# Kernel optimization log

Measured on AMD Instinct MI355X. Metric: run time of the kernel, lower is better.

Reference implementation:

```python
import jax, jax.numpy as jnp
import numpy as np

B, H, L = 8, 256, 8192

def setup_inputs() -> dict:
    key = jax.random.key(0)
    k1, k2, k3 = jax.random.split(key, 3)
    u = jax.random.normal(k1, (B, H, L), dtype=jnp.float32)
    K = jax.random.normal(k2, (H, L), dtype=jnp.float32)
    # D ~ uniform_ring with min=max=1.0, field='real' -> random signs on unit ring
    D = jnp.where(jax.random.uniform(k3, (H,)) < 0.5, -1.0, 1.0).astype(jnp.float32)
    return {"u": u, "K": K, "D": D}

def reference(u, K, D):
    # FFT-based circular long convolution per channel: y = ifft(fft(u) * fft(K)).real
    u_s = jnp.fft.fft(u, axis=-1)            # (B,H,L) complex
    k_s = jnp.fft.fft(K, axis=-1)            # (H,L)   complex
    y = jnp.fft.ifft(u_s * k_s[None], axis=-1).real  # (B,H,L)
    y = y + D[None, :, None] * u             # skip connection D*u
    y = jnp.tanh(y)
    return y
```

## Files before the change

### kernel.cpp

```cpp
#include <hip/hip_runtime.h>
#include <math.h>


#define LL 8192
#define NT 256
#define HH 256
#define TWO_PI 6.2831853071795864f
#define CP16 0.98078528040323f
#define SP16 0.19509032201613f
#define CP8  0.92387953251129f
#define SP8  0.38268343236509f

__device__ __forceinline__ int PHYS(int i) {
    return i ^ ((i >> 5) & 15) ^ (((i >> 8) & 1) << 4);
}
__device__ __forceinline__ float fast_tanh(float x) {
    float e = __expf(2.0f * x);
    return 1.0f - 2.0f / (e + 1.0f);
}

template<int JT>
__device__ __forceinline__ void fill_pyr_cs(float c0, float s0, float Er, float Ei,
                                            float* twr, float* twi) {
    const int off = (1 << JT) - 1;
    twr[off] = c0; twi[off] = s0;
    #pragma unroll
    for (int m = 1; m < (1 << JT); ++m) {
        const float pr = twr[off + m - 1], pi = twi[off + m - 1];
        twr[off + m] = pr * Er - pi * Ei;
        twi[off + m] = pr * Ei + pi * Er;
    }
    #pragma unroll
    for (int j = JT - 1; j >= 0; --j) {
        #pragma unroll
        for (int m = 0; m < (1 << j); ++m) {
            const float a = twr[(2 << j) - 1 + m], b = twi[(2 << j) - 1 + m];
            twr[(1 << j) - 1 + m] = a * a - b * b;
            twi[(1 << j) - 1 + m] = 2.0f * a * b;
        }
    }
}
template<int JT>
__device__ __forceinline__ void fill_pyr(float ang0, float Er, float Ei,
                                         float* twr, float* twi) {
    float s, c;
    __sincosf(ang0, &s, &c);
    fill_pyr_cs<JT>(c, s, Er, Ei, twr, twi);
}

template<int R2>
__device__ __forceinline__ void dif_apply(float* xr, float* xi,
                                          const float* twr, const float* twi) {
    #pragma unroll
    for (int j = R2 - 1; j >= 0; --j) {
        #pragma unroll
        for (int q = 0; q < (1 << (R2 - 1)); ++q) {
            const int mm = q & ((1 << j) - 1);
            const int m0 = ((q >> j) << (j + 1)) | mm;
            const int m1 = m0 + (1 << j);
            const float wr = twr[(1 << j) - 1 + mm], wi = twi[(1 << j) - 1 + mm];
            const float ar = xr[m0], ai = xi[m0], br = xr[m1], bi = xi[m1];
            xr[m0] = ar + br; xi[m0] = ai + bi;
            const float dr = ar - br, di = ai - bi;
            xr[m1] = dr * wr - di * wi;
            xi[m1] = dr * wi + di * wr;
        }
    }
}
template<int R2>
__device__ __forceinline__ void dit_apply(float* xr, float* xi,
                                          const float* twr, const float* twi) {
    #pragma unroll
    for (int j = 0; j < R2; ++j) {
        #pragma unroll
        for (int q = 0; q < (1 << (R2 - 1)); ++q) {
            const int mm = q & ((1 << j) - 1);
            const int m0 = ((q >> j) << (j + 1)) | mm;
            const int m1 = m0 + (1 << j);
            const float wr = twr[(1 << j) - 1 + mm], wi = twi[(1 << j) - 1 + mm];
            const float br = xr[m1] * wr - xi[m1] * wi;
            const float bi = xr[m1] * wi + xi[m1] * wr;
            const float ar = xr[m0], ai = xi[m0];
            xr[m0] = ar + br; xi[m0] = ai + bi;
            xr[m1] = ar - br; xi[m1] = ai - bi;
        }
    }
}

__device__ __forceinline__ void fwd_A(float* xr, float* xi, int tid,
                                      float* re, float* im) {
    float twr[31], twi[31];
    fill_pyr<4>(-(TWO_PI / 8192.0f) * (float)tid, CP16, -SP16, twr, twi);
    dif_apply<5>(xr, xi, twr, twi);
    #pragma unroll
    for (int m = 0; m < 32; ++m) {
        const int p = PHYS(tid + (m << 8));
        re[p] = xr[m]; im[p] = xi[m];
    }
}

__device__ __forceinline__ void fwd_B(int tid, float* re, float* im) {
    #pragma unroll
    for (int gg = 0; gg < 2; ++gg) {
        const int g = tid + (gg << 8);
        const int base = ((g >> 4) << 8) | (g & 15);
        float xr[16], xi[16], twr[15], twi[15];
        #pragma unroll
        for (int m = 0; m < 16; ++m) {
            const int p = PHYS(base + (m << 4));
            xr[m] = re[p]; xi[m] = im[p];
        }
        fill_pyr<3>(-(TWO_PI / 256.0f) * (float)(g & 15), CP8, -SP8, twr, twi);
        dif_apply<4>(xr, xi, twr, twi);
        #pragma unroll
        for (int m = 0; m < 16; ++m) {
            const int p = PHYS(base + (m << 4));
            re[p] = xr[m]; im[p] = xi[m];
        }
    }
}

__device__ __forceinline__ void inv_B(int tid, float* re, float* im) {
    #pragma unroll
    for (int gg = 0; gg < 2; ++gg) {
        const int g = tid + (gg << 8);
        const int base = ((g >> 4) << 8) | (g & 15);
        float xr[16], xi[16], twr[15], twi[15];
        #pragma unroll
        for (int m = 0; m < 16; ++m) {
            const int p = PHYS(base + (m << 4));
            xr[m] = re[p]; xi[m] = im[p];
        }
        fill_pyr<3>((TWO_PI / 256.0f) * (float)(g & 15), CP8, SP8, twr, twi);
        dit_apply<4>(xr, xi, twr, twi);
        #pragma unroll
        for (int m = 0; m < 16; ++m) {
            const int p = PHYS(base + (m << 4));
            re[p] = xr[m]; im[p] = xi[m];
        }
    }
}

__global__ __launch_bounds__(NT) void kfft_kernel(const float* __restrict__ K,
                                                  float2* __restrict__ Kf) {
    __shared__ float re[LL];
    __shared__ float im[LL];
    const int h = blockIdx.x;
    const int tid = threadIdx.x;
    const float* Kr = K + (size_t)h * LL;
    float xr[32], xi[32];
    #pragma unroll
    for (int m = 0; m < 32; ++m) {
        xr[m] = Kr[tid + (m << 8)];
        xi[m] = 0.0f;
    }
    fwd_A(xr, xi, tid, re, im);
    __syncthreads();
    fwd_B(tid, re, im);
    __syncthreads();
    #pragma unroll
    for (int gg = 0; gg < 2; ++gg) {
        const int base = (tid + (gg << 8)) << 4;
        float yr[16], yi[16], twr[15], twi[15];
        #pragma unroll
        for (int m = 0; m < 16; ++m) {
            const int p = PHYS(base + m);
            yr[m] = re[p]; yi[m] = im[p];
        }
        fill_pyr_cs<3>(1.0f, 0.0f, CP8, -SP8, twr, twi);
        dif_apply<4>(yr, yi, twr, twi);
        #pragma unroll
        for (int m = 0; m < 16; ++m) {
            const int p = PHYS(base + m);
            re[p] = yr[m]; im[p] = yi[m];
        }
    }
    __syncthreads();
    float2* outp = Kf + (size_t)h * LL;
    #pragma unroll
    for (int t = 0; t < 32; ++t) {
        const int lin = t * NT + tid;
        const int m = lin >> 9;
        const int i0 = lin & 511;
        const int p = PHYS((i0 << 4) | m);
        outp[lin] = make_float2(re[p], im[p]);
    }
}

__global__ __launch_bounds__(NT) void conv_kernel(const float* __restrict__ u,
                                                  const float2* __restrict__ Kf,
                                                  const float* __restrict__ D,
                                                  float* __restrict__ out) {
    __shared__ float re[LL];
    __shared__ float im[LL];
    const int tid = threadIdx.x;
    const int h = blockIdx.x & (HH - 1);
    const int pr_ = blockIdx.x >> 8;
    const size_t off0 = ((size_t)(pr_ * 2) * HH + h) * LL;
    const size_t off1 = off0 + (size_t)HH * LL;
    const float* u0 = u + off0;
    const float* u1 = u + off1;

    float xr[32], xi[32];
    #pragma unroll
    for (int m = 0; m < 32; ++m) {
        xr[m] = u0[tid + (m << 8)];
        xi[m] = u1[tid + (m << 8)];
    }
    fwd_A(xr, xi, tid, re, im);
    __syncthreads();
    fwd_B(tid, re, im);
    __syncthreads();

    const float2* kf = Kf + (size_t)h * LL;
    #pragma unroll
    for (int gg = 0; gg < 2; ++gg) {
        const int i0 = tid + (gg << 8);
        const int base = i0 << 4;
        float yr[16], yi[16], twr[15], twi[15];
        #pragma unroll
        for (int m = 0; m < 16; ++m) {
            const int p = PHYS(base + m);
            yr[m] = re[p]; yi[m] = im[p];
        }
        fill_pyr_cs<3>(1.0f, 0.0f, CP8, -SP8, twr, twi);
        dif_apply<4>(yr, yi, twr, twi);
        #pragma unroll
        for (int m = 0; m < 16; ++m) {
            const float2 w = kf[(m << 9) + i0];
            const float a = yr[m], b = yi[m];
            yr[m] = a * w.x - b * w.y;
            yi[m] = a * w.y + b * w.x;
        }
        fill_pyr_cs<3>(1.0f, 0.0f, CP8, SP8, twr, twi);
        dit_apply<4>(yr, yi, twr, twi);
        #pragma unroll
        for (int m = 0; m < 16; ++m) {
            const int p = PHYS(base + m);
            re[p] = yr[m]; im[p] = yi[m];
        }
    }
    __syncthreads();

    inv_B(tid, re, im);
    __syncthreads();

    {
        float twr[31], twi[31];
        #pragma unroll
        for (int m = 0; m < 32; ++m) {
            const int p = PHYS(tid + (m << 8));
            xr[m] = re[p]; xi[m] = im[p];
        }
        fill_pyr<4>((TWO_PI / 8192.0f) * (float)tid, CP16, SP16, twr, twi);
        dit_apply<5>(xr, xi, twr, twi);
    }
    const float dh = D[h];
    const float invN = 1.0f / (float)LL;
    float* o0 = out + off0;
    float* o1 = out + off1;
    #pragma unroll
    for (int m = 0; m < 32; ++m) {
        const int n = tid + (m << 8);
        o0[n] = fast_tanh(xr[m] * invN + dh * u0[n]);
        o1[n] = fast_tanh(xi[m] * invN + dh * u1[n]);
    }
}

extern "C" void kernel_launch(void* const* d_in, const int* in_sizes, int n_in,
                              void* d_out, int out_size, void* d_ws, size_t ws_size,
                              hipStream_t stream) {
    const float* u = (const float*)d_in[0];
    const float* K = (const float*)d_in[1];
    const float* D = (const float*)d_in[2];
    float* out = (float*)d_out;
    float2* Kf = (float2*)d_ws;

    kfft_kernel<<<dim3(HH), dim3(NT), 0, stream>>>(K, Kf);
    conv_kernel<<<dim3(4 * HH), dim3(NT), 0, stream>>>(u, Kf, D, out);
}
```

Baseline: 157.7 us.

## Fuse kernel FFT into conv kernel and fold skip term into spectrum

Removes the separate K-FFT kernel and workspace by having each conv block recompute the FFT of its channel's K in registers. The D*u skip connection and 1/N scaling are folded into the kernel spectrum (adding D to every bin), eliminating the second read of u in the epilogue. This trades extra redundant FFT compute per block and higher register pressure for less global memory traffic and one fewer launch.

```diff
diff --git a/kernel.cpp b/kernel.cpp
--- a/kernel.cpp
+++ b/kernel.cpp
@@ -98,7 +98,6 @@
         re[p] = xr[m]; im[p] = xi[m];
     }
 }
-
 __device__ __forceinline__ void fwd_B(int tid, float* re, float* im) {
     #pragma unroll
     for (int gg = 0; gg < 2; ++gg) {
@@ -119,7 +118,6 @@
         }
     }
 }
-
 __device__ __forceinline__ void inv_B(int tid, float* re, float* im) {
     #pragma unroll
     for (int gg = 0; gg < 2; ++gg) {
@@ -141,61 +139,51 @@
     }
 }
 
-__global__ __launch_bounds__(NT) void kfft_kernel(const float* __restrict__ K,
-                                                  float2* __restrict__ Kf) {
-    __shared__ float re[LL];
-    __shared__ float im[LL];
-    const int h = blockIdx.x;
-    const int tid = threadIdx.x;
-    const float* Kr = K + (size_t)h * LL;
-    float xr[32], xi[32];
-    #pragma unroll
-    for (int m = 0; m < 32; ++m) {
-        xr[m] = Kr[tid + (m << 8)];
-        xi[m] = 0.0f;
-    }
-    fwd_A(xr, xi, tid, re, im);
-    __syncthreads();
-    fwd_B(tid, re, im);
-    __syncthreads();
-    #pragma unroll
-    for (int gg = 0; gg < 2; ++gg) {
-        const int base = (tid + (gg << 8)) << 4;
-        float yr[16], yi[16], twr[15], twi[15];
-        #pragma unroll
-        for (int m = 0; m < 16; ++m) {
-            const int p = PHYS(base + m);
-            yr[m] = re[p]; yi[m] = im[p];
-        }
-        fill_pyr_cs<3>(1.0f, 0.0f, CP8, -SP8, twr, twi);
-        dif_apply<4>(yr, yi, twr, twi);
-        #pragma unroll
-        for (int m = 0; m < 16; ++m) {
-            const int p = PHYS(base + m);
-            re[p] = yr[m]; im[p] = yi[m];
-        }
-    }
-    __syncthreads();
-    float2* outp = Kf + (size_t)h * LL;
-    #pragma unroll
-    for (int t = 0; t < 32; ++t) {
-        const int lin = t * NT + tid;
-        const int m = lin >> 9;
-        const int i0 = lin & 511;
-        const int p = PHYS((i0 << 4) | m);
-        outp[lin] = make_float2(re[p], im[p]);
-    }
-}
-
-__global__ __launch_bounds__(NT) void conv_kernel(const float* __restrict__ u,
-                                                  const float2* __restrict__ Kf,
-                                                  const float* __restrict__ D,
-                                                  float* __restrict__ out) {
+__global__ __launch_bounds__(NT) void conv_fused(const float* __restrict__ u,
+                                                 const float* __restrict__ K,
+                                                 const float* __restrict__ D,
+                                                 float* __restrict__ out) {
     __shared__ float re[LL];
     __shared__ float im[LL];
     const int tid = threadIdx.x;
     const int h = blockIdx.x & (HH - 1);
     const int pr_ = blockIdx.x >> 8;
+
+    float kr[2][16], ki[2][16];
+    {
+        const float* Krow = K + (size_t)h * LL;
+        float ar[32], ai[32];
+        #pragma unroll
+        for (int m = 0; m < 32; ++m) {
+            ar[m] = Krow[tid + (m << 8)];
+            ai[m] = 0.0f;
+        }
+        fwd_A(ar, ai, tid, re, im);
+        __syncthreads();
+        fwd_B(tid, re, im);
+        __syncthreads();
+        const float dh = D[h];
+        const float invN = 1.0f / (float)LL;
+        #pragma unroll
+        for (int gg = 0; gg < 2; ++gg) {
+            const int base = (tid + (gg << 8)) << 4;
+            float yr[16], yi[16], twr[15], twi[15];
+            #pragma unroll
+            for (int m = 0; m < 16; ++m) {
+                const int p = PHYS(base + m);
+                yr[m] = re[p]; yi[m] = im[p];
+            }
+            fill_pyr_cs<3>(1.0f, 0.0f, CP8, -SP8, twr, twi);
+            dif_apply<4>(yr, yi, twr, twi);
+            #pragma unroll
+            for (int m = 0; m < 16; ++m) {
+                kr[gg][m] = (yr[m] + dh) * invN;
+                ki[gg][m] = yi[m] * invN;
+            }
+        }
+        __syncthreads();
+    }
+
     const size_t off0 = ((size_t)(pr_ * 2) * HH + h) * LL;
     const size_t off1 = off0 + (size_t)HH * LL;
     const float* u0 = u + off0;
@@ -212,11 +200,9 @@
     fwd_B(tid, re, im);
     __syncthreads();
 
-    const float2* kf = Kf + (size_t)h * LL;
     #pragma unroll
     for (int gg = 0; gg < 2; ++gg) {
-        const int i0 = tid + (gg << 8);
-        const int base = i0 << 4;
+        const int base = (tid + (gg << 8)) << 4;
         float yr[16], yi[16], twr[15], twi[15];
         #pragma unroll
         for (int m = 0; m < 16; ++m) {
@@ -227,10 +213,9 @@
         dif_apply<4>(yr, yi, twr, twi);
         #pragma unroll
         for (int m = 0; m < 16; ++m) {
-            const float2 w = kf[(m << 9) + i0];
             const float a = yr[m], b = yi[m];
-            yr[m] = a * w.x - b * w.y;
-            yi[m] = a * w.y + b * w.x;
+            yr[m] = a * kr[gg][m] - b * ki[gg][m];
+            yi[m] = a * ki[gg][m] + b * kr[gg][m];
         }
         fill_pyr_cs<3>(1.0f, 0.0f, CP8, SP8, twr, twi);
         dit_apply<4>(yr, yi, twr, twi);
@@ -255,15 +240,13 @@
         fill_pyr<4>((TWO_PI / 8192.0f) * (float)tid, CP16, SP16, twr, twi);
         dit_apply<5>(xr, xi, twr, twi);
     }
-    const float dh = D[h];
-    const float invN = 1.0f / (float)LL;
     float* o0 = out + off0;
     float* o1 = out + off1;
     #pragma unroll
     for (int m = 0; m < 32; ++m) {
         const int n = tid + (m << 8);
-        o0[n] = fast_tanh(xr[m] * invN + dh * u0[n]);
-        o1[n] = fast_tanh(xi[m] * invN + dh * u1[n]);
+        o0[n] = fast_tanh(xr[m]);
+        o1[n] = fast_tanh(xi[m]);
     }
 }
 
@@ -274,8 +257,6 @@
     const float* K = (const float*)d_in[1];
     const float* D = (const float*)d_in[2];
     float* out = (float*)d_out;
-    float2* Kf = (float2*)d_ws;
-
-    kfft_kernel<<<dim3(HH), dim3(NT), 0, stream>>>(K, Kf);
-    conv_kernel<<<dim3(4 * HH), dim3(NT), 0, stream>>>(u, Kf, D, out);
-}
+
+    conv_fused<<<dim3(4 * HH), dim3(NT), 0, stream>>>(u, K, D, out);
+}
```

New measurement: 178.2 us. +13.0%, slower.

## Prefetch kernel spectrum early and batch two FFT groups per pass

Applied to the files above, without the earlier changes.

The spectrum of K is now loaded into registers at kernel start, before the forward FFT, so global-load latency overlaps the FFT stages instead of stalling the pointwise multiply. The radix-16 stages in fwd_B, inv_B and the middle pass now load both groups first and compute both before storing, which gives more independent work per thread and shares one twiddle table (g&15 equals tid&15). launch_bounds is set to 2 blocks per CU. The extra 64 live registers for the prefetch plus the doubled working set raise register pressure and risk spills.

```diff
diff --git a/kernel.cpp b/kernel.cpp
--- a/kernel.cpp
+++ b/kernel.cpp
@@ -100,43 +100,55 @@
 }
 
 __device__ __forceinline__ void fwd_B(int tid, float* re, float* im) {
+    float xr[2][16], xi[2][16], twr[15], twi[15];
     #pragma unroll
     for (int gg = 0; gg < 2; ++gg) {
         const int g = tid + (gg << 8);
         const int base = ((g >> 4) << 8) | (g & 15);
-        float xr[16], xi[16], twr[15], twi[15];
         #pragma unroll
         for (int m = 0; m < 16; ++m) {
             const int p = PHYS(base + (m << 4));
-            xr[m] = re[p]; xi[m] = im[p];
-        }
-        fill_pyr<3>(-(TWO_PI / 256.0f) * (float)(g & 15), CP8, -SP8, twr, twi);
-        dif_apply<4>(xr, xi, twr, twi);
-        #pragma unroll
-        for (int m = 0; m < 16; ++m) {
-            const int p = PHYS(base + (m << 4));
-            re[p] = xr[m]; im[p] = xi[m];
-        }
-    }
-}
-
-__device__ __forceinline__ void inv_B(int tid, float* re, float* im) {
+            xr[gg][m] = re[p]; xi[gg][m] = im[p];
+        }
+    }
+    fill_pyr<3>(-(TWO_PI / 256.0f) * (float)(tid & 15), CP8, -SP8, twr, twi);
+    dif_apply<4>(xr[0], xi[0], twr, twi);
+    dif_apply<4>(xr[1], xi[1], twr, twi);
     #pragma unroll
     for (int gg = 0; gg < 2; ++gg) {
         const int g = tid + (gg << 8);
         const int base = ((g >> 4) << 8) | (g & 15);
-        float xr[16], xi[16], twr[15], twi[15];
         #pragma unroll
         for (int m = 0; m < 16; ++m) {
             const int p = PHYS(base + (m << 4));
-            xr[m] = re[p]; xi[m] = im[p];
-        }
-        fill_pyr<3>((TWO_PI / 256.0f) * (float)(g & 15), CP8, SP8, twr, twi);
-        dit_apply<4>(xr, xi, twr, twi);
+            re[p] = xr[gg][m]; im[p] = xi[gg][m];
+        }
+    }
+}
+
+__device__ __forceinline__ void inv_B(int tid, float* re, float* im) {
+    float xr[2][16], xi[2][16], twr[15], twi[15];
+    #pragma unroll
+    for (int gg = 0; gg < 2; ++gg) {
+        const int g = tid + (gg << 8);
+        const int base = ((g >> 4) << 8) | (g & 15);
         #pragma unroll
         for (int m = 0; m < 16; ++m) {
             const int p = PHYS(base + (m << 4));
-            re[p] = xr[m]; im[p] = xi[m];
+            xr[gg][m] = re[p]; xi[gg][m] = im[p];
+        }
+    }
+    fill_pyr<3>((TWO_PI / 256.0f) * (float)(tid & 15), CP8, SP8, twr, twi);
+    dit_apply<4>(xr[0], xi[0], twr, twi);
+    dit_apply<4>(xr[1], xi[1], twr, twi);
+    #pragma unroll
+    for (int gg = 0; gg < 2; ++gg) {
+        const int g = tid + (gg << 8);
+        const int base = ((g >> 4) << 8) | (g & 15);
+        #pragma unroll
+        for (int m = 0; m < 16; ++m) {
+            const int p = PHYS(base + (m << 4));
+            re[p] = xr[gg][m]; im[p] = xi[gg][m];
         }
     }
 }
@@ -187,10 +199,10 @@
     }
 }
 
-__global__ __launch_bounds__(NT) void conv_kernel(const float* __restrict__ u,
-                                                  const float2* __restrict__ Kf,
-                                                  const float* __restrict__ D,
-                                                  float* __restrict__ out) {
+__global__ __launch_bounds__(NT, 2) void conv_kernel(const float* __restrict__ u,
+                                                     const float2* __restrict__ Kf,
+                                                     const float* __restrict__ D,
+                                                     float* __restrict__ out) {
     __shared__ float re[LL];
     __shared__ float im[LL];
     const int tid = threadIdx.x;
@@ -207,37 +219,57 @@
         xr[m] = u0[tid + (m << 8)];
         xi[m] = u1[tid + (m << 8)];
     }
+    const float2* kf = Kf + (size_t)h * LL;
+    float kfr[2][16], kfi[2][16];
+    #pragma unroll
+    for (int gg = 0; gg < 2; ++gg) {
+        const int i0 = tid + (gg << 8);
+        #pragma unroll
+        for (int m = 0; m < 16; ++m) {
+            const float2 w = kf[(m << 9) + i0];
+            kfr[gg][m] = w.x; kfi[gg][m] = w.y;
+        }
+    }
+
     fwd_A(xr, xi, tid, re, im);
     __syncthreads();
     fwd_B(tid, re, im);
     __syncthreads();
 
-    const float2* kf = Kf + (size_t)h * LL;
-    #pragma unroll
-    for (int gg = 0; gg < 2; ++gg) {
-        const int i0 = tid + (gg << 8);
-        const int base = i0 << 4;
-        float yr[16], yi[16], twr[15], twi[15];
-        #pragma unroll
-        for (int m = 0; m < 16; ++m) {
-            const int p = PHYS(base + m);
-            yr[m] = re[p]; yi[m] = im[p];
+    {
+        float yr[2][16], yi[2][16], twr[15], twi[15];
+        #pragma unroll
+        for (int gg = 0; gg < 2; ++gg) {
+            const int base = (tid + (gg << 8)) << 4;
+            #pragma unroll
+            for (int m = 0; m < 16; ++m) {
+                const int p = PHYS(base + m);
+                yr[gg][m] = re[p]; yi[gg][m] = im[p];
+            }
         }
         fill_pyr_cs<3>(1.0f, 0.0f, CP8, -SP8, twr, twi);
-        dif_apply<4>(yr, yi, twr, twi);
-        #pragma unroll
-        for (int m = 0; m < 16; ++m) {
-            const float2 w = kf[(m << 9) + i0];
-            const float a = yr[m], b = yi[m];
-            yr[m] = a * w.x - b * w.y;
-            yi[m] = a * w.y + b * w.x;
+        dif_apply<4>(yr[0], yi[0], twr, twi);
+        dif_apply<4>(yr[1], yi[1], twr, twi);
+        #pragma unroll
+        for (int gg = 0; gg < 2; ++gg) {
+            #pragma unroll
+            for (int m = 0; m < 16; ++m) {
+                const float a = yr[gg][m], b = yi[gg][m];
+                yr[gg][m] = a * kfr[gg][m] - b * kfi[gg][m];
+                yi[gg][m] = a * kfi[gg][m] + b * kfr[gg][m];
+            }
         }
         fill_pyr_cs<3>(1.0f, 0.0f, CP8, SP8, twr, twi);
-        dit_apply<4>(yr, yi, twr, twi);
-        #pragma unroll
-        for (int m = 0; m < 16; ++m) {
-            const int p = PHYS(base + m);
-            re[p] = yr[m]; im[p] = yi[m];
+        dit_apply<4>(yr[0], yi[0], twr, twi);
+        dit_apply<4>(yr[1], yi[1], twr, twi);
+        #pragma unroll
+        for (int gg = 0; gg < 2; ++gg) {
+            const int base = (tid + (gg << 8)) << 4;
+            #pragma unroll
+            for (int m = 0; m < 16; ++m) {
+                const int p = PHYS(base + m);
+                re[p] = yr[gg][m]; im[p] = yi[gg][m];
+            }
         }
     }
     __syncthreads();
```

After: 217.0 us. 37.6% more time.

## Switch FFT to 512 threads with 16x16x32 radix split and fold D into kernel spectrum

Applied to the files above, without the earlier changes.

Restructures the 8192-point FFT from 256 threads doing radix-32/16/16 into 512 threads doing radix-16/16/32. The last radix-32 stage is split into a radix-16 pass plus a radix-2 step done through lane shuffles. The skip term D*u and the 1/N scaling are folded into the precomputed kernel spectrum, since the FFT of D*delta is constant D. This removes the re-read of u and a multiply from the epilogue. The swizzle is changed to match the new strides. Doubling the threads halves per-thread registers, which may improve occupancy, but it adds shuffles and the block still uses 64KB of LDS.

```diff
diff --git a/kernel.cpp b/kernel.cpp
--- a/kernel.cpp
+++ b/kernel.cpp
@@ -3,16 +3,14 @@
 
 
 #define LL 8192
-#define NT 256
+#define NT 512
 #define HH 256
 #define TWO_PI 6.2831853071795864f
-#define CP16 0.98078528040323f
-#define SP16 0.19509032201613f
 #define CP8  0.92387953251129f
 #define SP8  0.38268343236509f
 
 __device__ __forceinline__ int PHYS(int i) {
-    return i ^ ((i >> 5) & 15) ^ (((i >> 8) & 1) << 4);
+    return i ^ ((i >> 5) & 15) ^ ((((i >> 8) ^ (i >> 5)) & 1) << 4);
 }
 __device__ __forceinline__ float fast_tanh(float x) {
     float e = __expf(2.0f * x);
@@ -89,107 +87,93 @@
 
 __device__ __forceinline__ void fwd_A(float* xr, float* xi, int tid,
                                       float* re, float* im) {
-    float twr[31], twi[31];
-    fill_pyr<4>(-(TWO_PI / 8192.0f) * (float)tid, CP16, -SP16, twr, twi);
-    dif_apply<5>(xr, xi, twr, twi);
-    #pragma unroll
-    for (int m = 0; m < 32; ++m) {
-        const int p = PHYS(tid + (m << 8));
+    float twr[15], twi[15];
+    fill_pyr<3>(-(TWO_PI / 8192.0f) * (float)tid, CP8, -SP8, twr, twi);
+    dif_apply<4>(xr, xi, twr, twi);
+    #pragma unroll
+    for (int m = 0; m < 16; ++m) {
+        const int p = PHYS(tid + (m << 9));
         re[p] = xr[m]; im[p] = xi[m];
     }
 }
-
 __device__ __forceinline__ void fwd_B(int tid, float* re, float* im) {
-    #pragma unroll
-    for (int gg = 0; gg < 2; ++gg) {
-        const int g = tid + (gg << 8);
-        const int base = ((g >> 4) << 8) | (g & 15);
-        float xr[16], xi[16], twr[15], twi[15];
-        #pragma unroll
-        for (int m = 0; m < 16; ++m) {
-            const int p = PHYS(base + (m << 4));
-            xr[m] = re[p]; xi[m] = im[p];
-        }
-        fill_pyr<3>(-(TWO_PI / 256.0f) * (float)(g & 15), CP8, -SP8, twr, twi);
-        dif_apply<4>(xr, xi, twr, twi);
-        #pragma unroll
-        for (int m = 0; m < 16; ++m) {
-            const int p = PHYS(base + (m << 4));
-            re[p] = xr[m]; im[p] = xi[m];
-        }
-    }
-}
-
+    const int r_ = tid & 31;
+    const int base = ((tid >> 5) << 9) | r_;
+    float xr[16], xi[16], twr[15], twi[15];
+    #pragma unroll
+    for (int m = 0; m < 16; ++m) {
+        const int p = PHYS(base + (m << 5));
+        xr[m] = re[p]; xi[m] = im[p];
+    }
+    fill_pyr<3>(-(TWO_PI / 512.0f) * (float)r_, CP8, -SP8, twr, twi);
+    dif_apply<4>(xr, xi, twr, twi);
+    #pragma unroll
+    for (int m = 0; m < 16; ++m) {
+        const int p = PHYS(base + (m << 5));
+        re[p] = xr[m]; im[p] = xi[m];
+    }
+}
 __device__ __forceinline__ void inv_B(int tid, float* re, float* im) {
-    #pragma unroll
-    for (int gg = 0; gg < 2; ++gg) {
-        const int g = tid + (gg << 8);
-        const int base = ((g >> 4) << 8) | (g & 15);
-        float xr[16], xi[16], twr[15], twi[15];
-        #pragma unroll
-        for (int m = 0; m < 16; ++m) {
-            const int p = PHYS(base + (m << 4));
-            xr[m] = re[p]; xi[m] = im[p];
-        }
-        fill_pyr<3>((TWO_PI / 256.0f) * (float)(g & 15), CP8, SP8, twr, twi);
-        dit_apply<4>(xr, xi, twr, twi);
-        #pragma unroll
-        for (int m = 0; m < 16; ++m) {
-            const int p = PHYS(base + (m << 4));
-            re[p] = xr[m]; im[p] = xi[m];
-        }
+    const int r_ = tid & 31;
+    const int base = ((tid >> 5) << 9) | r_;
+    float xr[16], xi[16], twr[15], twi[15];
+    #pragma unroll
+    for (int m = 0; m < 16; ++m) {
+        const int p = PHYS(base + (m << 5));
+        xr[m] = re[p]; xi[m] = im[p];
+    }
+    fill_pyr<3>((TWO_PI / 512.0f) * (float)r_, CP8, SP8, twr, twi);
+    dit_apply<4>(xr, xi, twr, twi);
+    #pragma unroll
+    for (int m = 0; m < 16; ++m) {
+        const int p = PHYS(base + (m << 5));
+        re[p] = xr[m]; im[p] = xi[m];
     }
 }
 
 __global__ __launch_bounds__(NT) void kfft_kernel(const float* __restrict__ K,
+                                                  const float* __restrict__ D,
                                                   float2* __restrict__ Kf) {
     __shared__ float re[LL];
     __shared__ float im[LL];
     const int h = blockIdx.x;
     const int tid = threadIdx.x;
     const float* Kr = K + (size_t)h * LL;
-    float xr[32], xi[32];
-    #pragma unroll
-    for (int m = 0; m < 32; ++m) {
-        xr[m] = Kr[tid + (m << 8)];
+    float xr[16], xi[16];
+    #pragma unroll
+    for (int m = 0; m < 16; ++m) {
+        xr[m] = Kr[tid + (m << 9)];
         xi[m] = 0.0f;
     }
     fwd_A(xr, xi, tid, re, im);
     __syncthreads();
     fwd_B(tid, re, im);
     __syncthreads();
-    #pragma unroll
-    for (int gg = 0; gg < 2; ++gg) {
-        const int base = (tid + (gg << 8)) << 4;
-        float yr[16], yi[16], twr[15], twi[15];
-        #pragma unroll
-        for (int m = 0; m < 16; ++m) {
-            const int p = PHYS(base + m);
-            yr[m] = re[p]; yi[m] = im[p];
-        }
-        fill_pyr_cs<3>(1.0f, 0.0f, CP8, -SP8, twr, twi);
-        dif_apply<4>(yr, yi, twr, twi);
-        #pragma unroll
-        for (int m = 0; m < 16; ++m) {
-            const int p = PHYS(base + m);
-            re[p] = yr[m]; im[p] = yi[m];
-        }
-    }
-    __syncthreads();
+    const int par = tid & 1;
+    const int base = ((tid >> 1) << 5) | par;
+    float yr[16], yi[16], twr[15], twi[15];
+    #pragma unroll
+    for (int m = 0; m < 16; ++m) {
+        const int p = PHYS(base + (m << 1));
+        yr[m] = re[p]; yi[m] = im[p];
+    }
+    fill_pyr<3>(-(TWO_PI / 32.0f) * (float)par, CP8, -SP8, twr, twi);
+    dif_apply<4>(yr, yi, twr, twi);
+    const float dh = D[h];
+    const float invN = 1.0f / (float)LL;
     float2* outp = Kf + (size_t)h * LL;
     #pragma unroll
-    for (int t = 0; t < 32; ++t) {
-        const int lin = t * NT + tid;
-        const int m = lin >> 9;
-        const int i0 = lin & 511;
-        const int p = PHYS((i0 << 4) | m);
-        outp[lin] = make_float2(re[p], im[p]);
+    for (int m = 0; m < 16; ++m) {
+        const float ar = yr[m], ai = yi[m];
+        const float br = __shfl_xor(ar, 1), bi = __shfl_xor(ai, 1);
+        const float sr = par ? (br - ar) : (ar + br);
+        const float si = par ? (bi - ai) : (ai + bi);
+        outp[(m << 9) + tid] = make_float2((sr + dh) * invN, si * invN);
     }
 }
 
 __global__ __launch_bounds__(NT) void conv_kernel(const float* __restrict__ u,
                                                   const float2* __restrict__ Kf,
-                                                  const float* __restrict__ D,
                                                   float* __restrict__ out) {
     __shared__ float re[LL];
     __shared__ float im[LL];
@@ -201,42 +185,52 @@
     const float* u0 = u + off0;
     const float* u1 = u + off1;
 
-    float xr[32], xi[32];
-    #pragma unroll
-    for (int m = 0; m < 32; ++m) {
-        xr[m] = u0[tid + (m << 8)];
-        xi[m] = u1[tid + (m << 8)];
+    float xr[16], xi[16];
+    #pragma unroll
+    for (int m = 0; m < 16; ++m) {
+        xr[m] = u0[tid + (m << 9)];
+        xi[m] = u1[tid + (m << 9)];
     }
     fwd_A(xr, xi, tid, re, im);
     __syncthreads();
     fwd_B(tid, re, im);
     __syncthreads();
 
-    const float2* kf = Kf + (size_t)h * LL;
-    #pragma unroll
-    for (int gg = 0; gg < 2; ++gg) {
-        const int i0 = tid + (gg << 8);
-        const int base = i0 << 4;
+    {
+        const int par = tid & 1;
+        const int base = ((tid >> 1) << 5) | par;
+        const float2* kf = Kf + (size_t)h * LL;
+        float kwr[16], kwi[16];
+        #pragma unroll
+        for (int m = 0; m < 16; ++m) {
+            const float2 w = kf[(m << 9) + tid];
+            kwr[m] = w.x; kwi[m] = w.y;
+        }
         float yr[16], yi[16], twr[15], twi[15];
         #pragma unroll
         for (int m = 0; m < 16; ++m) {
-            const int p = PHYS(base + m);
+            const int p = PHYS(base + (m << 1));
             yr[m] = re[p]; yi[m] = im[p];
         }
-        fill_pyr_cs<3>(1.0f, 0.0f, CP8, -SP8, twr, twi);
+        fill_pyr<3>(-(TWO_PI / 32.0f) * (float)par, CP8, -SP8, twr, twi);
         dif_apply<4>(yr, yi, twr, twi);
         #pragma unroll
         for (int m = 0; m < 16; ++m) {
-            const float2 w = kf[(m << 9) + i0];
-            const float a = yr[m], b = yi[m];
-            yr[m] = a * w.x - b * w.y;
-            yi[m] = a * w.y + b * w.x;
-        }
-        fill_pyr_cs<3>(1.0f, 0.0f, CP8, SP8, twr, twi);
+            const float ar = yr[m], ai = yi[m];
+            const float br = __shfl_xor(ar, 1), bi = __shfl_xor(ai, 1);
+            const float sr = par ? (br - ar) : (ar + br);
+            const float si = par ? (bi - ai) : (ai + bi);
+            const float mr = sr * kwr[m] - si * kwi[m];
+            const float mi = sr * kwi[m] + si * kwr[m];
+            const float qr = __shfl_xor(mr, 1), qi = __shfl_xor(mi, 1);
+            yr[m] = par ? (qr - mr) : (mr + qr);
+            yi[m] = par ? (qi - mi) : (mi + qi);
+        }
+        fill_pyr<3>((TWO_PI / 32.0f) * (float)par, CP8, SP8, twr, twi);
         dit_apply<4>(yr, yi, twr, twi);
         #pragma unroll
         for (int m = 0; m < 16; ++m) {
-            const int p = PHYS(base + m);
+            const int p = PHYS(base + (m << 1));
             re[p] = yr[m]; im[p] = yi[m];
         }
     }
@@ -246,24 +240,22 @@
     __syncthreads();
 
     {
-        float twr[31], twi[31];
-        #pragma unroll
-        for (int m = 0; m < 32; ++m) {
-            const int p = PHYS(tid + (m << 8));
+        float twr[15], twi[15];
+        #pragma unroll
+        for (int m = 0; m < 16; ++m) {
+            const int p = PHYS(tid + (m << 9));
             xr[m] = re[p]; xi[m] = im[p];
         }
-        fill_pyr<4>((TWO_PI / 8192.0f) * (float)tid, CP16, SP16, twr, twi);
-        dit_apply<5>(xr, xi, twr, twi);
-    }
-    const float dh = D[h];
-    const float invN = 1.0f / (float)LL;
+        fill_pyr<3>((TWO_PI / 8192.0f) * (float)tid, CP8, SP8, twr, twi);
+        dit_apply<4>(xr, xi, twr, twi);
+    }
     float* o0 = out + off0;
     float* o1 = out + off1;
     #pragma unroll
-    for (int m = 0; m < 32; ++m) {
-        const int n = tid + (m << 8);
-        o0[n] = fast_tanh(xr[m] * invN + dh * u0[n]);
-        o1[n] = fast_tanh(xi[m] * invN + dh * u1[n]);
+    for (int m = 0; m < 16; ++m) {
+        const int n = tid + (m << 9);
+        o0[n] = fast_tanh(xr[m]);
+        o1[n] = fast_tanh(xi[m]);
     }
 }
 
@@ -276,6 +268,6 @@
     float* out = (float*)d_out;
     float2* Kf = (float2*)d_ws;
 
-    kfft_kernel<<<dim3(HH), dim3(NT), 0, stream>>>(K, Kf);
-    conv_kernel<<<dim3(4 * HH), dim3(NT), 0, stream>>>(u, Kf, D, out);
-}
+    kfft_kernel<<<dim3(HH), dim3(NT), 0, stream>>>(K, D, Kf);
+    conv_kernel<<<dim3(4 * HH), dim3(NT), 0, stream>>>(u, Kf, out);
+}
```

Result: no change. 160.5 us (+1.8%).
